# Performance work log

Measured on AMD Instinct MI355X. Metric: run time of the kernel, lower is better.

## Reference

```python
import jax, jax.numpy as jnp
import numpy as np
import math

SR = 48000
HOP = 480
NH = 6
MEL_CH = 128
CHUNK = 256


def _lin_interp(x, out_len):
    # torch F.interpolate(mode='linear', align_corners=False) along last axis
    T = x.shape[-1]
    scale = T / out_len
    pos = (jnp.arange(out_len, dtype=jnp.float32) + 0.5) * scale - 0.5
    pos = jnp.clip(pos, 0.0, T - 1)
    i0 = jnp.floor(pos).astype(jnp.int32)
    i1 = jnp.minimum(i0 + 1, T - 1)
    w = (pos - i0.astype(jnp.float32))
    return x[..., i0] * (1.0 - w) + x[..., i1] * w


def _conv1d(x, w, b, pad):
    y = jax.lax.conv_general_dilated(x, w, (1,), [(pad, pad)],
                                     dimension_numbers=('NCH', 'OIH', 'NCH'))
    return y + b[None, :, None]


def _wrapped_cumsum(x, chunk=CHUNK):
    # faithful chunked phase-wrap cumsum: carry_{i+1} = fmod(total_i + carry_i, 1)
    B, C, T = x.shape
    n = T // chunk
    xc = x.reshape(B, C, n, chunk)
    cum = jnp.cumsum(xc, axis=-1)            # per-chunk cumsum [B,C,n,chunk]
    totals = jnp.moveaxis(cum[..., -1], -1, 0)  # [n,B,C]

    def step(carry, t):
        new = jnp.fmod(carry + t, 1.0)
        return new, carry  # emit carry *before* this chunk

    carry0 = jnp.zeros((B, C), dtype=x.dtype)
    _, carries = jax.lax.scan(step, carry0, totals)
    carries = jnp.moveaxis(carries, 0, -1)   # [B,C,n]
    out = jnp.fmod(cum + carries[..., None], 1.0)
    return out.reshape(B, C, T)


def setup_inputs() -> dict:
    key = jax.random.key(0)
    ks = jax.random.split(key, 10)
    B, T = 4, 2000
    T_AUD = T * HOP
    f0 = jax.random.uniform(ks[0], (B, T), jnp.float32, 0.0, 500.0)
    mel = jax.random.normal(ks[1], (B, MEL_CH, T), jnp.float32)
    noise = jax.random.normal(ks[2], (B, 1, T_AUD), jnp.float32)
    conv1_w = jax.random.normal(ks[3], (32, 1 + MEL_CH, 5), jnp.float32) * 0.05
    conv1_b = jax.random.normal(ks[4], (32,), jnp.float32) * 0.05
    conv2_w = jax.random.normal(ks[5], (NH, 32, 1), jnp.float32) * 0.05
    conv2_b = jax.random.normal(ks[6], (NH,), jnp.float32) * 0.05
    amp_logscale = -jnp.log(jnp.arange(1, NH + 1, dtype=jnp.float32))
    phase_offset = jax.random.normal(ks[7], (NH,), jnp.float32) * 0.1
    log_noise_voiced = jnp.asarray(math.log(0.003), jnp.float32)
    log_noise_unvoiced = jnp.asarray(math.log(0.003), jnp.float32)
    return dict(f0=f0, mel=mel, noise=noise, conv1_w=conv1_w, conv1_b=conv1_b,
                conv2_w=conv2_w, conv2_b=conv2_b, amp_logscale=amp_logscale,
                phase_offset=phase_offset, log_noise_voiced=log_noise_voiced,
                log_noise_unvoiced=log_noise_unvoiced)


def reference(f0, mel, noise, conv1_w, conv1_b, conv2_w, conv2_b,
              amp_logscale, phase_offset, log_noise_voiced, log_noise_unvoiced):
    f0 = f0[:, None, :]                                   # [B,1,T]
    T = f0.shape[-1]
    k = jnp.arange(1, NH + 1, dtype=jnp.float32)[None, :, None]

    # mel+f0 conditioned amplitude predictor (mel already at f0 frame rate)
    h = _conv1d(jnp.concatenate([f0, mel], axis=1), conv1_w, conv1_b, pad=2)
    amp_mod = _conv1d(jax.nn.silu(h), conv2_w, conv2_b, pad=0)  # [B,NH,T]

    T_aud = T * HOP
    f0_up = _lin_interp(f0, T_aud)                        # [B,1,T_aud]
    phase_inc = f0_up / SR
    base_phase = _wrapped_cumsum(phase_inc) * (2.0 * math.pi)

    offset = phase_offset[None, :, None]
    harmonics = jnp.sin(k * base_phase + offset * (2.0 * math.pi))
    harmonics = harmonics * jnp.exp(amp_logscale)[None, :, None]

    amp_mod_up = _lin_interp(amp_mod, T_aud)
    harmonics = harmonics * (2.0 * jax.nn.sigmoid(amp_mod_up))

    nyquist = SR / 2.0
    voiced_mask = (f0_up > 1.0).astype(jnp.float32)
    aa_mask = jax.nn.sigmoid((nyquist - k * f0_up) / (nyquist * 0.05))
    harmonics = harmonics * (aa_mask * voiced_mask)

    noise_amp = voiced_mask * jnp.exp(log_noise_voiced) + \
                (1.0 - voiced_mask) * jnp.exp(log_noise_unvoiced)
    noise_out = noise * noise_amp
    return jnp.concatenate([harmonics, noise_out], axis=1)  # [B,NH+1,T_aud]
```

## Files before the change

### kernel.cpp

```cpp
#include <hip/hip_runtime.h>
#include <math.h>

#define NH      6
#define T_IN    2000
#define T_AUD   960000
#define NB      4
#define C_IN    129
#define C_MID   32
#define CSPLIT  3
#define NC_PER  43
#define SPLIT_STRIDE (NB * C_MID * T_IN)

__global__ void k_conv1(const float* __restrict__ f0, const float* __restrict__ mel,
                        const float* __restrict__ w1, float* __restrict__ hpart) {
    const int t0  = blockIdx.x * 256;
    const int b   = blockIdx.y >> 2;
    const int o0  = (blockIdx.y & 3) * 8;
    const int z   = blockIdx.z;
    const int cbase = z * NC_PER;
    const int tid = threadIdx.x;

    __shared__ float xl[NC_PER][264];

    for (int idx = tid; idx < NC_PER * 66; idx += 256) {
        const int r = idx / 66;
        const int j = idx - r * 66;
        const int c = cbase + r;
        const float* row = (c == 0) ? (f0 + b * T_IN)
                                    : (mel + ((size_t)(b * 128 + (c - 1))) * T_IN);
        const int gt = t0 - 4 + j * 4;
        float4 v;
        if (gt >= 0 && gt + 3 < T_IN) {
            v = *(const float4*)(row + gt);
        } else {
            v.x = (gt + 0 >= 0 && gt + 0 < T_IN) ? row[gt + 0] : 0.0f;
            v.y = (gt + 1 >= 0 && gt + 1 < T_IN) ? row[gt + 1] : 0.0f;
            v.z = (gt + 2 >= 0 && gt + 2 < T_IN) ? row[gt + 2] : 0.0f;
            v.w = (gt + 3 >= 0 && gt + 3 < T_IN) ? row[gt + 3] : 0.0f;
        }
        *(float4*)(&xl[r][j * 4]) = v;
    }
    __syncthreads();

    float acc[8];
    #pragma unroll
    for (int oo = 0; oo < 8; ++oo) acc[oo] = 0.0f;

    for (int c = 0; c < NC_PER; ++c) {
        const float x0 = xl[c][tid + 2];
        const float x1 = xl[c][tid + 3];
        const float x2 = xl[c][tid + 4];
        const float x3 = xl[c][tid + 5];
        const float x4 = xl[c][tid + 6];
        const int cg = cbase + c;
        #pragma unroll
        for (int oo = 0; oo < 8; ++oo) {
            const float* wp = w1 + (size_t)(o0 + oo) * (C_IN * 5) + cg * 5;
            acc[oo] = fmaf(wp[0], x0, acc[oo]);
            acc[oo] = fmaf(wp[1], x1, acc[oo]);
            acc[oo] = fmaf(wp[2], x2, acc[oo]);
            acc[oo] = fmaf(wp[3], x3, acc[oo]);
            acc[oo] = fmaf(wp[4], x4, acc[oo]);
        }
    }

    const int t = t0 + tid;
    if (t < T_IN) {
        #pragma unroll
        for (int oo = 0; oo < 8; ++oo)
            hpart[(size_t)z * SPLIT_STRIDE + ((size_t)(b * C_MID + o0 + oo)) * T_IN + t] = acc[oo];
    }
}

__global__ void k_conv2(const float* __restrict__ hpart, const float* __restrict__ b1,
                        const float* __restrict__ w2, const float* __restrict__ b2,
                        float* __restrict__ amp) {
    const int g = blockIdx.x * 256 + threadIdx.x;
    if (g >= NB * NH * T_IN) return;
    const int b = g / (NH * T_IN);
    const int r = g - b * (NH * T_IN);
    const int h = r / T_IN;
    const int t = r - h * T_IN;
    float acc = b2[h];
    #pragma unroll
    for (int o = 0; o < C_MID; ++o) {
        const size_t base = ((size_t)(b * C_MID + o)) * T_IN + t;
        float v = hpart[base] + hpart[SPLIT_STRIDE + base] + hpart[2 * SPLIT_STRIDE + base] + b1[o];
        const float sg = __builtin_amdgcn_rcpf(1.0f + __expf(-v));
        acc = fmaf(w2[h * C_MID + o], v * sg, acc);
    }
    amp[g] = acc;
}

__global__ void k_prefix(const float* __restrict__ f0, float* __restrict__ Pf) {
    const int b   = blockIdx.x;
    const int tid = threadIdx.x;
    const float* f0b = f0 + b * T_IN;

    double loc[8];
    double c = 0.0;
    const int base = tid * 8;
    #pragma unroll
    for (int j = 0; j < 8; ++j) {
        const int idx = base + j;
        loc[j] = c;
        if (idx < T_IN - 1) c += (double)f0b[idx] + (double)f0b[idx + 1];
    }
    __shared__ double part[256];
    part[tid] = c;
    __syncthreads();
    double run = c;
    for (int d = 1; d < 256; d <<= 1) {
        const double tadd = (tid >= d) ? part[tid - d] : 0.0;
        __syncthreads();
        run += tadd;
        part[tid] = run;
        __syncthreads();
    }
    const double excl  = run - c;
    const double base0 = 240.0 * (double)f0b[0];
    #pragma unroll
    for (int j = 0; j < 8; ++j) {
        const int idx = base + j;
        if (idx < T_IN) {
            const double P = (base0 + 240.0 * (excl + loc[j])) * (1.0 / 48000.0);
            Pf[b * T_IN + idx] = (float)(P - floor(P));
        }
    }
}

__global__ __launch_bounds__(256) void k_main(
        const float* __restrict__ f0, const float* __restrict__ noise,
        const float* __restrict__ amp, const float* __restrict__ Pf,
        const float* __restrict__ amp_logscale, const float* __restrict__ phase_offset,
        const float* __restrict__ lnv, const float* __restrict__ lnu,
        float* __restrict__ out) {
    const int b   = blockIdx.y;
    const int tid = threadIdx.x;
    const int s0  = blockIdx.x * 1024;
    const int t0  = s0 + tid * 4;

    __shared__ float sf0[6];
    __shared__ float sPf[4];
    __shared__ float sam[NH][5];
    __shared__ float sasc[NH], soff[NH], snv, snu;

    const int ulo  = (s0 - 240) < 0 ? 0 : (s0 - 240);
    int i_lo = (unsigned)ulo / 480u;
    if (i_lo > 1998) i_lo = 1998;

    const float* f0b = f0 + b * T_IN;
    const float* Pfb = Pf + b * T_IN;

    if (tid < 6) {
        int idx = i_lo + tid; if (idx > 1999) idx = 1999;
        sf0[tid] = f0b[idx];
    } else if (tid >= 8 && tid < 12) {
        int idx = i_lo + (tid - 8); if (idx > 1999) idx = 1999;
        sPf[tid - 8] = Pfb[idx];
    } else if (tid >= 16 && tid < 46) {
        const int h  = (tid - 16) / 5;
        const int jj = (tid - 16) - h * 5;
        int idx = i_lo + jj; if (idx > 1999) idx = 1999;
        sam[h][jj] = amp[((size_t)(b * NH + h)) * T_IN + idx];
    } else if (tid >= 48 && tid < 54) {
        sasc[tid - 48] = __expf(amp_logscale[tid - 48]);
    } else if (tid >= 56 && tid < 62) {
        soff[tid - 56] = phase_offset[tid - 56];
    } else if (tid == 62) {
        snv = __expf(lnv[0]);
    } else if (tid == 63) {
        snu = __expf(lnu[0]);
    }
    __syncthreads();

    if (t0 >= T_AUD) return;

    const float inv48k = 1.0f / 48000.0f;
    float ph[4], wd[4], f0f[4], voiced[4];
    int li[4];
    #pragma unroll
    for (int j = 0; j < 4; ++j) {
        const int t = t0 + j;
        const int u = (t - 240) < 0 ? 0 : (t - 240);
        int i = (unsigned)u / 480u;
        if (i > 1998) i = 1998;
        li[j] = i - i_lo;
        const int m = t - i * 480 - 240;
        const int n = m + 1;
        const float nf = (float)n;
        const float Wn = (n <= 0) ? 0.0f
                       : ((n <= 480) ? nf * nf * (1.0f / 960.0f) : nf - 240.0f);
        const float fa = sf0[li[j]];
        const float fd = sf0[li[j] + 1] - fa;
        const float pr = sPf[li[j]] + (nf * fa + fd * Wn) * inv48k;
        ph[j] = pr - floorf(pr);

        float w = ((float)m + 0.5f) * (1.0f / 480.0f);
        w = w < 0.0f ? 0.0f : (w > 1.0f ? 1.0f : w);
        wd[j] = w;
        f0f[j] = fmaf(fd, w, fa);
        voiced[j] = (f0f[j] > 1.0f) ? 1.0f : 0.0f;
    }

    const size_t outb = (size_t)b * 7 * T_AUD;
    #pragma unroll
    for (int h = 0; h < NH; ++h) {
        const float kf = (float)(h + 1);
        const float ascale = sasc[h];
        const float off = soff[h];
        float r[4];
        #pragma unroll
        for (int j = 0; j < 4; ++j) {
            const float a0 = sam[h][li[j]];
            const float am = fmaf(sam[h][li[j] + 1] - a0, wd[j], a0);
            const float sig = __builtin_amdgcn_rcpf(1.0f + __expf(-am));
            const float arg = kf * ph[j] + off;
            const float fr  = arg - floorf(arg);
            const float sn  = __builtin_amdgcn_sinf(fr);
            const float aa  = __builtin_amdgcn_rcpf(
                1.0f + __expf(-(24000.0f - kf * f0f[j]) * (1.0f / 1200.0f)));
            r[j] = sn * ascale * (2.0f * sig) * (aa * voiced[j]);
        }
        float4 res; res.x = r[0]; res.y = r[1]; res.z = r[2]; res.w = r[3];
        *(float4*)(out + outb + (size_t)h * T_AUD + t0) = res;
    }

    const float4 nz = *(const float4*)(noise + (size_t)b * T_AUD + t0);
    float4 no;
    no.x = nz.x * (voiced[0] > 0.0f ? snv : snu);
    no.y = nz.y * (voiced[1] > 0.0f ? snv : snu);
    no.z = nz.z * (voiced[2] > 0.0f ? snv : snu);
    no.w = nz.w * (voiced[3] > 0.0f ? snv : snu);
    *(float4*)(out + outb + (size_t)6 * T_AUD + t0) = no;
}

extern "C" void kernel_launch(void* const* d_in, const int* in_sizes, int n_in,
                              void* d_out, int out_size, void* d_ws, size_t ws_size,
                              hipStream_t stream) {
    const float* f0   = (const float*)d_in[0];
    const float* mel  = (const float*)d_in[1];
    const float* nois = (const float*)d_in[2];
    const float* w1   = (const float*)d_in[3];
    const float* b1   = (const float*)d_in[4];
    const float* w2   = (const float*)d_in[5];
    const float* b2   = (const float*)d_in[6];
    const float* alog = (const float*)d_in[7];
    const float* poff = (const float*)d_in[8];
    const float* lnv  = (const float*)d_in[9];
    const float* lnu  = (const float*)d_in[10];
    float* out = (float*)d_out;

    float* hpart = (float*)d_ws;
    float* amp   = (float*)((char*)d_ws + 3072000);
    float* Pfrac = (float*)((char*)d_ws + 3264000);

    k_conv1<<<dim3(8, 16, CSPLIT), 256, 0, stream>>>(f0, mel, w1, hpart);
    k_conv2<<<dim3((NB * NH * T_IN + 255) / 256), 256, 0, stream>>>(hpart, b1, w2, b2, amp);
    k_prefix<<<dim3(NB), 256, 0, stream>>>(f0, Pfrac);
    k_main<<<dim3((T_AUD + 1023) / 1024, NB), 256, 0, stream>>>(
        f0, nois, amp, Pfrac, alog, poff, lnv, lnu, out);
}
```

Baseline: 190.8 us.

## Fuse conv2 and phase prefix scan into main synthesis kernel

Removes the separate conv2 and prefix-scan kernels. Each main block now recomputes the SiLU and 1x1 conv for its few frames from the conv1 partial sums, and rebuilds the phase prefix by reducing f0 up to its start frame. This cuts two launches and the intermediate buffers, in exchange for redundant per-block work and an extra barrier stage before synthesis.

New measurement: 188.7 us. Within noise of the previous version (-1.1%).

```diff
diff --git a/kernel.cpp b/kernel.cpp
--- a/kernel.cpp
+++ b/kernel.cpp
@@ -72,66 +72,11 @@
     }
 }
 
-__global__ void k_conv2(const float* __restrict__ hpart, const float* __restrict__ b1,
-                        const float* __restrict__ w2, const float* __restrict__ b2,
-                        float* __restrict__ amp) {
-    const int g = blockIdx.x * 256 + threadIdx.x;
-    if (g >= NB * NH * T_IN) return;
-    const int b = g / (NH * T_IN);
-    const int r = g - b * (NH * T_IN);
-    const int h = r / T_IN;
-    const int t = r - h * T_IN;
-    float acc = b2[h];
-    #pragma unroll
-    for (int o = 0; o < C_MID; ++o) {
-        const size_t base = ((size_t)(b * C_MID + o)) * T_IN + t;
-        float v = hpart[base] + hpart[SPLIT_STRIDE + base] + hpart[2 * SPLIT_STRIDE + base] + b1[o];
-        const float sg = __builtin_amdgcn_rcpf(1.0f + __expf(-v));
-        acc = fmaf(w2[h * C_MID + o], v * sg, acc);
-    }
-    amp[g] = acc;
-}
-
-__global__ void k_prefix(const float* __restrict__ f0, float* __restrict__ Pf) {
-    const int b   = blockIdx.x;
-    const int tid = threadIdx.x;
-    const float* f0b = f0 + b * T_IN;
-
-    double loc[8];
-    double c = 0.0;
-    const int base = tid * 8;
-    #pragma unroll
-    for (int j = 0; j < 8; ++j) {
-        const int idx = base + j;
-        loc[j] = c;
-        if (idx < T_IN - 1) c += (double)f0b[idx] + (double)f0b[idx + 1];
-    }
-    __shared__ double part[256];
-    part[tid] = c;
-    __syncthreads();
-    double run = c;
-    for (int d = 1; d < 256; d <<= 1) {
-        const double tadd = (tid >= d) ? part[tid - d] : 0.0;
-        __syncthreads();
-        run += tadd;
-        part[tid] = run;
-        __syncthreads();
-    }
-    const double excl  = run - c;
-    const double base0 = 240.0 * (double)f0b[0];
-    #pragma unroll
-    for (int j = 0; j < 8; ++j) {
-        const int idx = base + j;
-        if (idx < T_IN) {
-            const double P = (base0 + 240.0 * (excl + loc[j])) * (1.0 / 48000.0);
-            Pf[b * T_IN + idx] = (float)(P - floor(P));
-        }
-    }
-}
-
-__global__ __launch_bounds__(256) void k_main(
+__global__ __launch_bounds__(256) void k_main2(
         const float* __restrict__ f0, const float* __restrict__ noise,
-        const float* __restrict__ amp, const float* __restrict__ Pf,
+        const float* __restrict__ hpart,
+        const float* __restrict__ b1, const float* __restrict__ w2,
+        const float* __restrict__ b2,
         const float* __restrict__ amp_logscale, const float* __restrict__ phase_offset,
         const float* __restrict__ lnv, const float* __restrict__ lnu,
         float* __restrict__ out) {
@@ -140,37 +85,67 @@
     const int s0  = blockIdx.x * 1024;
     const int t0  = s0 + tid * 4;
 
-    __shared__ float sf0[6];
-    __shared__ float sPf[4];
-    __shared__ float sam[NH][5];
-    __shared__ float sasc[NH], soff[NH], snv, snu;
+    __shared__ float  sf0[6];
+    __shared__ float  sPf[4];
+    __shared__ float  smid[C_MID][5];
+    __shared__ float  sam[NH][5];
+    __shared__ float  sasc[NH], soff[NH], snv, snu;
+    __shared__ double swsum[4];
 
     const int ulo  = (s0 - 240) < 0 ? 0 : (s0 - 240);
     int i_lo = (unsigned)ulo / 480u;
     if (i_lo > 1998) i_lo = 1998;
 
     const float* f0b = f0 + b * T_IN;
-    const float* Pfb = Pf + b * T_IN;
+
+    double S = 0.0;
+    for (int j = tid; j < i_lo; j += 256)
+        S += (double)f0b[j] + (double)f0b[j + 1];
+    #pragma unroll
+    for (int d = 32; d >= 1; d >>= 1) S += __shfl_down(S, d, 64);
+    if ((tid & 63) == 0) swsum[tid >> 6] = S;
 
     if (tid < 6) {
         int idx = i_lo + tid; if (idx > 1999) idx = 1999;
         sf0[tid] = f0b[idx];
-    } else if (tid >= 8 && tid < 12) {
-        int idx = i_lo + (tid - 8); if (idx > 1999) idx = 1999;
-        sPf[tid - 8] = Pfb[idx];
-    } else if (tid >= 16 && tid < 46) {
-        const int h  = (tid - 16) / 5;
-        const int jj = (tid - 16) - h * 5;
+    } else if (tid >= 8 && tid < 14) {
+        sasc[tid - 8] = __expf(amp_logscale[tid - 8]);
+    } else if (tid >= 16 && tid < 22) {
+        soff[tid - 16] = phase_offset[tid - 16];
+    } else if (tid == 22) {
+        snv = __expf(lnv[0]);
+    } else if (tid == 23) {
+        snu = __expf(lnu[0]);
+    } else if (tid >= 32 && tid < 32 + C_MID * 5) {
+        const int r  = tid - 32;
+        const int o  = r / 5;
+        const int jj = r - o * 5;
         int idx = i_lo + jj; if (idx > 1999) idx = 1999;
-        sam[h][jj] = amp[((size_t)(b * NH + h)) * T_IN + idx];
-    } else if (tid >= 48 && tid < 54) {
-        sasc[tid - 48] = __expf(amp_logscale[tid - 48]);
-    } else if (tid >= 56 && tid < 62) {
-        soff[tid - 56] = phase_offset[tid - 56];
-    } else if (tid == 62) {
-        snv = __expf(lnv[0]);
-    } else if (tid == 63) {
-        snu = __expf(lnu[0]);
+        const size_t base = ((size_t)(b * C_MID + o)) * T_IN + idx;
+        const float v = hpart[base] + hpart[SPLIT_STRIDE + base]
+                      + hpart[2 * SPLIT_STRIDE + base] + b1[o];
+        smid[o][jj] = v * __builtin_amdgcn_rcpf(1.0f + __expf(-v));
+    }
+    __syncthreads();
+
+    if (tid < NH * 5) {
+        const int h  = tid / 5;
+        const int jj = tid - h * 5;
+        float a = b2[h];
+        #pragma unroll
+        for (int o = 0; o < C_MID; ++o)
+            a = fmaf(w2[h * C_MID + o], smid[o][jj], a);
+        sam[h][jj] = a;
+    }
+    if (tid == 32) {
+        double P = 240.0 * (double)f0b[0]
+                 + 240.0 * (swsum[0] + swsum[1] + swsum[2] + swsum[3]);
+        #pragma unroll
+        for (int k = 0; k < 4; ++k) {
+            const double q = P * (1.0 / 48000.0);
+            sPf[k] = (float)(q - floor(q));
+            P += 240.0 * ((double)sf0[k] + (double)sf0[k + 1]);
+        }
     }
     __syncthreads();
 
@@ -252,12 +227,8 @@
     float* out = (float*)d_out;
 
     float* hpart = (float*)d_ws;
-    float* amp   = (float*)((char*)d_ws + 3072000);
-    float* Pfrac = (float*)((char*)d_ws + 3264000);
 
     k_conv1<<<dim3(8, 16, CSPLIT), 256, 0, stream>>>(f0, mel, w1, hpart);
-    k_conv2<<<dim3((NB * NH * T_IN + 255) / 256), 256, 0, stream>>>(hpart, b1, w2, b2, amp);
-    k_prefix<<<dim3(NB), 256, 0, stream>>>(f0, Pfrac);
-    k_main<<<dim3((T_AUD + 1023) / 1024, NB), 256, 0, stream>>>(
-        f0, nois, amp, Pfrac, alog, poff, lnv, lnu, out);
+    k_main2<<<dim3((T_AUD + 1023) / 1024, NB), 256, 0, stream>>>(
+        f0, nois, hpart, b1, w2, b2, alog, poff, lnv, lnu, out);
 }
```
